# Optimization experiments

Hardware: AMD Instinct MI355X
Metric: run time of the kernel (lower is better)

Reference implementation:

```python
import jax, jax.numpy as jnp
import numpy as np
import math

E = 256          # embed_dim
H = 8            # num_heads
DH = E // H      # head_dim = 32
Q_LEN = 65536
KV_LEN = 65536
K_NBR = 16       # max_memory_len (neighbors per query)


def setup_inputs() -> dict:
    key = jax.random.key(0)
    ks = jax.random.split(key, 8)
    query = jax.random.normal(ks[0], (Q_LEN, E), dtype=jnp.float32)
    key_t = jax.random.normal(ks[1], (KV_LEN, E), dtype=jnp.float32)
    value = jax.random.normal(ks[2], (KV_LEN, E), dtype=jnp.float32)
    index_pair = jax.random.randint(ks[3], (Q_LEN, K_NBR), 0, KV_LEN, dtype=jnp.int64 if jax.config.jax_enable_x64 else jnp.int32)
    # learned params (xavier-ish init for in_proj, zero biases)
    lim = math.sqrt(6.0 / (3 * E + E))
    in_proj_weight = jax.random.uniform(ks[4], (3 * E, E), minval=-lim, maxval=lim, dtype=jnp.float32)
    in_proj_bias = jnp.zeros((3 * E,), dtype=jnp.float32)
    lim2 = math.sqrt(1.0 / E)
    out_proj_weight = jax.random.uniform(ks[5], (E, E), minval=-lim2, maxval=lim2, dtype=jnp.float32)
    out_proj_bias = jnp.zeros((E,), dtype=jnp.float32)
    return {
        "query": query, "key": key_t, "value": value, "index_pair": index_pair,
        "in_proj_weight": in_proj_weight, "in_proj_bias": in_proj_bias,
        "out_proj_weight": out_proj_weight, "out_proj_bias": out_proj_bias,
    }


def reference(query, key, value, index_pair, in_proj_weight, in_proj_bias, out_proj_weight, out_proj_bias):
    tq = query.shape[0]
    # input projections (split rows of packed in_proj_weight)
    q = query @ in_proj_weight[:E].T + in_proj_bias[:E]
    k = key @ in_proj_weight[E:2 * E].T + in_proj_bias[E:2 * E]
    v = value @ in_proj_weight[2 * E:].T + in_proj_bias[2 * E:]
    q = q.reshape(tq, H, DH) / math.sqrt(DH)   # [Q,H,Dh]
    k = k.reshape(-1, H, DH)                    # [N,H,Dh]
    v = v.reshape(-1, H, DH)
    invalid = index_pair < 0                    # [Q,K]
    all_invalid = jnp.all(invalid, axis=-1)     # [Q]
    safe_pair = jnp.clip(index_pair, 0)
    gathered_k = k[safe_pair]                   # [Q,K,H,Dh]
    gathered_v = v[safe_pair]
    weights = jnp.einsum('qhd,qkhd->qkh', q, gathered_k)  # [Q,K,H]
    neg_inf = jnp.asarray(-jnp.inf, weights.dtype)
    weights = jnp.where(invalid[..., None], neg_inf, weights)
    weights = jnp.where(all_invalid[:, None, None], jnp.zeros((), weights.dtype), weights)
    weights = jax.nn.softmax(weights, axis=1)
    weights = jnp.where(invalid[..., None], jnp.zeros((), weights.dtype), weights)
    out = jnp.einsum('qkh,qkhd->qhd', weights, gathered_v).reshape(tq, E)
    out = out @ out_proj_weight.T + out_proj_bias
    return out, weights.sum(axis=-1) / H
```

## Files before the change

### kernel.cpp

```cpp
#include <hip/hip_runtime.h>
#include <hip/hip_fp16.h>

#define QLEN   65536
#define EDIM   256

typedef _Float16 half8 __attribute__((ext_vector_type(8)));
typedef float    f32x4 __attribute__((ext_vector_type(4)));

static const size_t WQKV_OFF = 0;
static const size_t WOUT_OFF = 768u * 256u * 2u;
static const size_t Q_OFF    = WOUT_OFF + 256u * 256u * 2u;
static const size_t K_OFF    = Q_OFF + (size_t)QLEN * EDIM * 2u;
static const size_t V_OFF    = K_OFF + (size_t)QLEN * EDIM * 2u;
static const size_t A_OFF    = V_OFF + (size_t)QLEN * EDIM * 2u;

__global__ void prep_weights(const float* __restrict__ wqkv,
                             const float* __restrict__ wout,
                             __half* __restrict__ dst)
{
  int g = (blockIdx.x * blockDim.x + threadIdx.x) * 4;
  float4 f;
  if (g < 768 * 256) f = *(const float4*)(wqkv + g);
  else               f = *(const float4*)(wout + (g - 768 * 256));
  union { __half h[4]; uint2 u; } c;
  c.h[0] = __float2half(f.x); c.h[1] = __float2half(f.y);
  c.h[2] = __float2half(f.z); c.h[3] = __float2half(f.w);
  *(uint2*)(dst + g) = c.u;
}

template<bool A_F32, bool OUT_F16>
__global__ __launch_bounds__(256)
void gemm_e256(const void* __restrict__ Ain,
               const __half* __restrict__ W,
               const float* __restrict__ bias,
               float scale,
               void* __restrict__ Outp)
{
  __shared__ __half As[128][40];
  __shared__ __half Bs[128][40];
  const int tid  = threadIdx.x;
  const int lane = tid & 63;
  const int wid  = tid >> 6;
  const int wr   = wid >> 1, wc = wid & 1;
  const int gm   = blockIdx.x * 128;
  const int gn   = blockIdx.y * 128;

  f32x4 acc[4][4] = {};

  const int sr = tid >> 1;
  const int sk = (tid & 1) * 16;

  const int fr = lane & 15;
  const int fo = (lane >> 4) * 8;

  for (int kc = 0; kc < 8; ++kc) {
    __syncthreads();
    if (A_F32) {
      const float* A   = (const float*)Ain;
      const float* src = A + (size_t)(gm + sr) * 256 + kc * 32 + sk;
      union { __half h[16]; uint4 u[2]; } t;
      #pragma unroll
      for (int u = 0; u < 4; ++u) {
        float4 f = ((const float4*)src)[u];
        t.h[u*4+0] = __float2half(f.x); t.h[u*4+1] = __float2half(f.y);
        t.h[u*4+2] = __float2half(f.z); t.h[u*4+3] = __float2half(f.w);
      }
      *(uint4*)&As[sr][sk]     = t.u[0];
      *(uint4*)&As[sr][sk + 8] = t.u[1];
    } else {
      const __half* A  = (const __half*)Ain;
      const uint4* src = (const uint4*)(A + (size_t)(gm + sr) * 256 + kc * 32 + sk);
      *(uint4*)&As[sr][sk]     = src[0];
      *(uint4*)&As[sr][sk + 8] = src[1];
    }
    {
      const uint4* src = (const uint4*)(W + (size_t)(gn + sr) * 256 + kc * 32 + sk);
      *(uint4*)&Bs[sr][sk]     = src[0];
      *(uint4*)&Bs[sr][sk + 8] = src[1];
    }
    __syncthreads();

    half8 af[4], bf[4];
    #pragma unroll
    for (int i = 0; i < 4; ++i) af[i] = *(const half8*)&As[wr*64 + i*16 + fr][fo];
    #pragma unroll
    for (int j = 0; j < 4; ++j) bf[j] = *(const half8*)&Bs[wc*64 + j*16 + fr][fo];
    #pragma unroll
    for (int i = 0; i < 4; ++i)
      #pragma unroll
      for (int j = 0; j < 4; ++j)
        acc[i][j] = __builtin_amdgcn_mfma_f32_16x16x32_f16(af[i], bf[j], acc[i][j], 0, 0, 0);
  }

  const int fq = lane >> 4;
  #pragma unroll
  for (int j = 0; j < 4; ++j) {
    const int col = gn + wc*64 + j*16 + fr;
    const float bj = bias[col];
    #pragma unroll
    for (int i = 0; i < 4; ++i) {
      const int row0 = gm + wr*64 + i*16 + fq*4;
      #pragma unroll
      for (int rr = 0; rr < 4; ++rr) {
        const float v = (acc[i][j][rr] + bj) * scale;
        if (OUT_F16) ((__half*)Outp)[(size_t)(row0 + rr) * 256 + col] = __float2half(v);
        else         ((float*) Outp)[(size_t)(row0 + rr) * 256 + col] = v;
      }
    }
  }
}

__global__ __launch_bounds__(256)
void attn_local(const __half* __restrict__ qws, const __half* __restrict__ kws,
                const __half* __restrict__ vws, const int* __restrict__ idxp,
                __half* __restrict__ attn, float* __restrict__ wsum)
{
  const int tid  = threadIdx.x;
  const int lane = tid & 63;
  const int wid  = tid >> 6;
  const int q    = blockIdx.x * 4 + wid;
  const int col  = lane * 4;

  union U2 { uint2 u; __half h[4]; };

  U2 qu; qu.u = *(const uint2*)(qws + (size_t)q * 256 + col);
  const float q0 = __half2float(qu.h[0]), q1 = __half2float(qu.h[1]),
              q2 = __half2float(qu.h[2]), q3 = __half2float(qu.h[3]);

  int myidx = 0;
  if (lane < 16) myidx = idxp[(size_t)q * 16 + lane];

  float logit[16];
  U2 vk[16];
  #pragma unroll
  for (int n = 0; n < 16; ++n) {
    const int kvi = __shfl(myidx, n);
    float p;
    if (kvi >= 0) {
      U2 ku; ku.u = *(const uint2*)(kws + (size_t)kvi * 256 + col);
      vk[n].u     = *(const uint2*)(vws + (size_t)kvi * 256 + col);
      p = q0 * __half2float(ku.h[0]) + q1 * __half2float(ku.h[1])
        + q2 * __half2float(ku.h[2]) + q3 * __half2float(ku.h[3]);
      p += __shfl_xor(p, 1);
      p += __shfl_xor(p, 2);
      p += __shfl_xor(p, 4);
    } else {
      p = -__builtin_inff();
      vk[n].u = make_uint2(0u, 0u);
    }
    logit[n] = p;
  }

  float m = logit[0];
  #pragma unroll
  for (int n = 1; n < 16; ++n) m = fmaxf(m, logit[n]);
  const bool allinv = (m < -1e37f);

  float w[16]; float ssum = 0.f;
  #pragma unroll
  for (int n = 0; n < 16; ++n) {
    const float e = allinv ? 0.f : __expf(logit[n] - m);
    w[n] = e; ssum += e;
  }
  const float inv = allinv ? 0.f : (1.0f / ssum);

  float a0 = 0.f, a1 = 0.f, a2 = 0.f, a3 = 0.f;
  #pragma unroll
  for (int n = 0; n < 16; ++n) {
    const float wn = w[n] * inv;
    w[n] = wn;
    a0 += wn * __half2float(vk[n].h[0]);
    a1 += wn * __half2float(vk[n].h[1]);
    a2 += wn * __half2float(vk[n].h[2]);
    a3 += wn * __half2float(vk[n].h[3]);
  }

  U2 o; o.h[0] = __float2half(a0); o.h[1] = __float2half(a1);
        o.h[2] = __float2half(a2); o.h[3] = __float2half(a3);
  *(uint2*)(attn + (size_t)q * 256 + col) = o.u;

  float wsr = 0.f;
  #pragma unroll
  for (int n = 0; n < 16; ++n) {
    float t = w[n];
    t += __shfl_xor(t, 8);
    t += __shfl_xor(t, 16);
    t += __shfl_xor(t, 32);
    if (lane == n) wsr = t;
  }
  if (lane < 16) wsum[(size_t)q * 16 + lane] = wsr * 0.125f;
}

extern "C" void kernel_launch(void* const* d_in, const int* in_sizes, int n_in,
                              void* d_out, int out_size, void* d_ws, size_t ws_size,
                              hipStream_t stream)
{
  const float* query = (const float*)d_in[0];
  const float* key   = (const float*)d_in[1];
  const float* value = (const float*)d_in[2];
  const int*   idxp  = (const int*)  d_in[3];
  const float* wqkv  = (const float*)d_in[4];
  const float* bqkv  = (const float*)d_in[5];
  const float* wout  = (const float*)d_in[6];
  const float* bout  = (const float*)d_in[7];
  float* out = (float*)d_out;

  char* ws   = (char*)d_ws;
  __half* Wh = (__half*)(ws + WQKV_OFF);
  __half* qh = (__half*)(ws + Q_OFF);
  __half* kh = (__half*)(ws + K_OFF);
  __half* vh = (__half*)(ws + V_OFF);
  __half* ah = (__half*)(ws + A_OFF);

  prep_weights<<<256, 256, 0, stream>>>(wqkv, wout, Wh);

  dim3 ggrid(QLEN / 128, 2);
  const float qscale = 0.17677669529663687f;
  gemm_e256<true,  true ><<<ggrid, 256, 0, stream>>>(query, Wh,             bqkv,       qscale, qh);
  gemm_e256<true,  true ><<<ggrid, 256, 0, stream>>>(key,   Wh + 256*256,   bqkv + 256, 1.0f,   kh);
  gemm_e256<true,  true ><<<ggrid, 256, 0, stream>>>(value, Wh + 512*256,   bqkv + 512, 1.0f,   vh);

  attn_local<<<QLEN / 4, 256, 0, stream>>>(qh, kh, vh, idxp, ah, out + (size_t)QLEN * EDIM);

  gemm_e256<false, false><<<ggrid, 256, 0, stream>>>(ah, Wh + 768*256, bout, 1.0f, out);
}
```

Baseline: 492.2 us.

## Widen GEMM tiles to full N, double-buffer LDS, merge QKV projections into one launch

The GEMM now uses a 128x256 output tile with 512 threads, so each A row tile is read and converted from fp32 once rather than twice across two N-blocks. Shared-memory tiles are double-buffered, with global loads for the next K chunk issued before the MFMA work and stored afterwards, which removes one barrier per iteration and overlaps load latency with compute. The three Q/K/V projections are merged into a single launch selected by blockIdx.y, which saves launch overhead and gives a larger grid. In exchange, LDS use and register pressure go up, which may lower occupancy.

```diff
diff --git a/kernel.cpp b/kernel.cpp
--- a/kernel.cpp
+++ b/kernel.cpp
@@ -29,74 +29,113 @@
 }
 
 template<bool A_F32, bool OUT_F16>
-__global__ __launch_bounds__(256)
-void gemm_e256(const void* __restrict__ Ain,
-               const __half* __restrict__ W,
-               const float* __restrict__ bias,
-               float scale,
-               void* __restrict__ Outp)
-{
-  __shared__ __half As[128][40];
-  __shared__ __half Bs[128][40];
+__global__ __launch_bounds__(512)
+void gemm_e256v2(const void* __restrict__ A0, const void* __restrict__ A1,
+                 const void* __restrict__ A2,
+                 const __half* __restrict__ Wbase, const float* __restrict__ bias,
+                 float scale0,
+                 void* __restrict__ O0, void* __restrict__ O1, void* __restrict__ O2)
+{
+  __shared__ __half As[2][128][40];
+  __shared__ __half Bs[2][256][40];
+
+  const int y = blockIdx.y;
+  const void* Ain  = (y == 0) ? A0 : (y == 1) ? A1 : A2;
+  void*       Outp = (y == 0) ? O0 : (y == 1) ? O1 : O2;
+  const __half* W  = Wbase + (size_t)y * 256 * 256;
+  const float* bp  = bias + y * 256;
+  const float scale = (y == 0) ? scale0 : 1.0f;
+
   const int tid  = threadIdx.x;
   const int lane = tid & 63;
   const int wid  = tid >> 6;
-  const int wr   = wid >> 1, wc = wid & 1;
+  const int wr   = wid >> 2;
+  const int wc   = wid & 3;
   const int gm   = blockIdx.x * 128;
-  const int gn   = blockIdx.y * 128;
-
-  f32x4 acc[4][4] = {};
-
-  const int sr = tid >> 1;
-  const int sk = (tid & 1) * 16;
+
+  const int ar = tid >> 2, ac = (tid & 3) * 8;
+  const int br = tid >> 1, bc = (tid & 1) * 16;
 
   const int fr = lane & 15;
   const int fo = (lane >> 4) * 8;
-
-  for (int kc = 0; kc < 8; ++kc) {
+  const int fq = lane >> 4;
+
+  f32x4 acc[4][4] = {};
+
+  float4 ra0, ra1;
+  uint4  ua;
+  uint4  rb0, rb1;
+
+  if (A_F32) {
+    const float* src = (const float*)Ain + (size_t)(gm + ar) * 256 + ac;
+    ra0 = ((const float4*)src)[0];
+    ra1 = ((const float4*)src)[1];
+    union { __half h[8]; uint4 u; } t;
+    t.h[0]=__float2half(ra0.x); t.h[1]=__float2half(ra0.y);
+    t.h[2]=__float2half(ra0.z); t.h[3]=__float2half(ra0.w);
+    t.h[4]=__float2half(ra1.x); t.h[5]=__float2half(ra1.y);
+    t.h[6]=__float2half(ra1.z); t.h[7]=__float2half(ra1.w);
+    *(uint4*)&As[0][ar][ac] = t.u;
+  } else {
+    const __half* src = (const __half*)Ain + (size_t)(gm + ar) * 256 + ac;
+    *(uint4*)&As[0][ar][ac] = *(const uint4*)src;
+  }
+  {
+    const __half* src = W + (size_t)br * 256 + bc;
+    *(uint4*)&Bs[0][br][bc]     = ((const uint4*)src)[0];
+    *(uint4*)&Bs[0][br][bc + 8] = ((const uint4*)src)[1];
+  }
+
+  int cur = 0;
+  #pragma unroll
+  for (int kc = 0; kc < 8; ++kc, cur ^= 1) {
+    if (kc < 7) {
+      if (A_F32) {
+        const float* src = (const float*)Ain + (size_t)(gm + ar) * 256 + (kc + 1) * 32 + ac;
+        ra0 = ((const float4*)src)[0];
+        ra1 = ((const float4*)src)[1];
+      } else {
+        const __half* src = (const __half*)Ain + (size_t)(gm + ar) * 256 + (kc + 1) * 32 + ac;
+        ua = *(const uint4*)src;
+      }
+      const __half* src = W + (size_t)br * 256 + (kc + 1) * 32 + bc;
+      rb0 = ((const uint4*)src)[0];
+      rb1 = ((const uint4*)src)[1];
+    }
+
     __syncthreads();
-    if (A_F32) {
-      const float* A   = (const float*)Ain;
-      const float* src = A + (size_t)(gm + sr) * 256 + kc * 32 + sk;
-      union { __half h[16]; uint4 u[2]; } t;
-      #pragma unroll
-      for (int u = 0; u < 4; ++u) {
-        float4 f = ((const float4*)src)[u];
-        t.h[u*4+0] = __float2half(f.x); t.h[u*4+1] = __float2half(f.y);
-        t.h[u*4+2] = __float2half(f.z); t.h[u*4+3] = __float2half(f.w);
-      }
-      *(uint4*)&As[sr][sk]     = t.u[0];
-      *(uint4*)&As[sr][sk + 8] = t.u[1];
-    } else {
-      const __half* A  = (const __half*)Ain;
-      const uint4* src = (const uint4*)(A + (size_t)(gm + sr) * 256 + kc * 32 + sk);
-      *(uint4*)&As[sr][sk]     = src[0];
-      *(uint4*)&As[sr][sk + 8] = src[1];
-    }
-    {
-      const uint4* src = (const uint4*)(W + (size_t)(gn + sr) * 256 + kc * 32 + sk);
-      *(uint4*)&Bs[sr][sk]     = src[0];
-      *(uint4*)&Bs[sr][sk + 8] = src[1];
-    }
-    __syncthreads();
 
     half8 af[4], bf[4];
     #pragma unroll
-    for (int i = 0; i < 4; ++i) af[i] = *(const half8*)&As[wr*64 + i*16 + fr][fo];
-    #pragma unroll
-    for (int j = 0; j < 4; ++j) bf[j] = *(const half8*)&Bs[wc*64 + j*16 + fr][fo];
+    for (int i = 0; i < 4; ++i) af[i] = *(const half8*)&As[cur][wr*64 + i*16 + fr][fo];
+    #pragma unroll
+    for (int j = 0; j < 4; ++j) bf[j] = *(const half8*)&Bs[cur][wc*64 + j*16 + fr][fo];
     #pragma unroll
     for (int i = 0; i < 4; ++i)
       #pragma unroll
       for (int j = 0; j < 4; ++j)
         acc[i][j] = __builtin_amdgcn_mfma_f32_16x16x32_f16(af[i], bf[j], acc[i][j], 0, 0, 0);
-  }
-
-  const int fq = lane >> 4;
+
+    if (kc < 7) {
+      if (A_F32) {
+        union { __half h[8]; uint4 u; } t;
+        t.h[0]=__float2half(ra0.x); t.h[1]=__float2half(ra0.y);
+        t.h[2]=__float2half(ra0.z); t.h[3]=__float2half(ra0.w);
+        t.h[4]=__float2half(ra1.x); t.h[5]=__float2half(ra1.y);
+        t.h[6]=__float2half(ra1.z); t.h[7]=__float2half(ra1.w);
+        *(uint4*)&As[cur ^ 1][ar][ac] = t.u;
+      } else {
+        *(uint4*)&As[cur ^ 1][ar][ac] = ua;
+      }
+      *(uint4*)&Bs[cur ^ 1][br][bc]     = rb0;
+      *(uint4*)&Bs[cur ^ 1][br][bc + 8] = rb1;
+    }
+  }
+
   #pragma unroll
   for (int j = 0; j < 4; ++j) {
-    const int col = gn + wc*64 + j*16 + fr;
-    const float bj = bias[col];
+    const int col = wc*64 + j*16 + fr;
+    const float bj = bp[col];
     #pragma unroll
     for (int i = 0; i < 4; ++i) {
       const int row0 = gm + wr*64 + i*16 + fq*4;
@@ -214,13 +253,13 @@
 
   prep_weights<<<256, 256, 0, stream>>>(wqkv, wout, Wh);
 
-  dim3 ggrid(QLEN / 128, 2);
   const float qscale = 0.17677669529663687f;
-  gemm_e256<true,  true ><<<ggrid, 256, 0, stream>>>(query, Wh,             bqkv,       qscale, qh);
-  gemm_e256<true,  true ><<<ggrid, 256, 0, stream>>>(key,   Wh + 256*256,   bqkv + 256, 1.0f,   kh);
-  gemm_e256<true,  true ><<<ggrid, 256, 0, stream>>>(value, Wh + 512*256,   bqkv + 512, 1.0f,   vh);
+
+  gemm_e256v2<true, true><<<dim3(QLEN / 128, 3), 512, 0, stream>>>(
+      query, key, value, Wh, bqkv, qscale, qh, kh, vh);
 
   attn_local<<<QLEN / 4, 256, 0, stream>>>(qh, kh, vh, idxp, ah, out + (size_t)QLEN * EDIM);
 
-  gemm_e256<false, false><<<ggrid, 256, 0, stream>>>(ah, Wh + 768*256, bout, 1.0f, out);
-}
+  gemm_e256v2<false, false><<<dim3(QLEN / 128, 1), 512, 0, stream>>>(
+      ah, ah, ah, Wh + 768 * 256, bout, 1.0f, out, out, out);
+}
```

After: 452.1 us. 8.2% less time.
